# Kernel optimization log

Hardware: AMD Instinct MI355X
Metric: run time of the kernel (lower is better)

## Reference

```python
import jax, jax.numpy as jnp
import numpy as np

B, S, DIN, DK, DV = 8, 2048, 1024, 1024, 1024


def setup_inputs() -> dict:
    key = jax.random.key(0)
    ks = jax.random.split(key, 9)
    s_in = 1.0 / np.sqrt(DIN)
    return {
        "query": jax.random.normal(ks[0], (B, S, DIN), jnp.float32),
        "key_": jax.random.normal(ks[1], (B, S, DIN), jnp.float32),
        "value": jax.random.normal(ks[2], (B, S, DIN), jnp.float32),
        "Wq_w": jax.random.uniform(ks[3], (DK, DIN), jnp.float32, -s_in, s_in),
        "Wq_b": jax.random.uniform(ks[4], (DK,), jnp.float32, -s_in, s_in),
        "Wk_w": jax.random.uniform(ks[5], (DK, DIN), jnp.float32, -s_in, s_in),
        "Wk_b": jax.random.uniform(ks[6], (DK,), jnp.float32, -s_in, s_in),
        "Wv_w": jax.random.uniform(ks[7], (DV, DIN), jnp.float32, -s_in, s_in),
        "Wv_b": jax.random.uniform(ks[8], (DV,), jnp.float32, -s_in, s_in),
    }


def reference(query, key_, value, Wq_w, Wq_b, Wk_w, Wk_b, Wv_w, Wv_b):
    # Linear projections: x @ W.T + b (torch nn.Linear convention)
    Q = jnp.einsum('bsd,kd->bsk', query, Wq_w) + Wq_b   # [B,S,DK]
    K = jnp.einsum('bsd,kd->bsk', key_, Wk_w) + Wk_b    # [B,S,DK]
    V = jnp.einsum('bsd,vd->bsv', value, Wv_w) + Wv_b   # [B,S,DV]
    scale = 1.0 / jnp.sqrt(jnp.asarray(Q.shape[-1], Q.dtype))
    scores = jnp.einsum('bqk,bsk->bqs', Q, K) * scale   # [B,S,S]
    attn = jax.nn.softmax(scores, axis=-1)
    return jnp.einsum('bqs,bsv->bqv', attn, V)          # [B,S,DV]
```

## Files before the change

### kernel.cpp

```cpp
#include <hip/hip_runtime.h>

typedef unsigned short u16;
typedef float    f32x4  __attribute__((ext_vector_type(4)));
typedef __bf16   bf16x8 __attribute__((ext_vector_type(8)));
typedef u16      u16x4  __attribute__((ext_vector_type(4)));
typedef u16      u16x8  __attribute__((ext_vector_type(8)));

#define NB   8
#define NS   2048
#define ND   1024

__device__ __forceinline__ u16 f2bf(float x) {
    union { float f; unsigned u; } v; v.f = x;
    unsigned r = v.u + 0x7fffu + ((v.u >> 16) & 1u);
    return (u16)(r >> 16);
}
__device__ __forceinline__ float bf2f(u16 x) {
    union { unsigned u; float f; } v; v.u = ((unsigned)x) << 16;
    return v.f;
}

__global__ __launch_bounds__(256) void cvt_f32_bf16(const float* __restrict__ in,
                                                    u16* __restrict__ out, int n4) {
    int i = blockIdx.x * 256 + threadIdx.x;
    if (i >= n4) return;
    f32x4 v = ((const f32x4*)in)[i];
    u16x4 o;
    o[0] = f2bf(v[0]); o[1] = f2bf(v[1]); o[2] = f2bf(v[2]); o[3] = f2bf(v[3]);
    ((u16x4*)out)[i] = o;
}

template<int OUT_BF16, int BIAS>
__global__ __launch_bounds__(256, 2)
void gemm_bt_kernel(const u16* __restrict__ A, long long sA, int lda,
                    const u16* __restrict__ B, long long sB, int ldb,
                    void* __restrict__ Cv, long long sC, int ldc,
                    const float* __restrict__ bias, int K)
{
    __shared__ alignas(16) u16 ldsA[128 * 32];
    __shared__ alignas(16) u16 ldsB[128 * 32];
    const int z = blockIdx.z;
    A += sA * z;
    B += sB * z;
    const int t = threadIdx.x;
    const int w = t >> 6, l = t & 63;
    const int row0 = blockIdx.y * 128, col0 = blockIdx.x * 128;
    const int wr = (w >> 1) << 6, wc = (w & 1) << 6;

    f32x4 acc[4][4] = {};
    const int lr = l & 15, lk = (l >> 4) << 3;

    for (int kt = 0; kt < K; kt += 32) {
#pragma unroll
        for (int i = 0; i < 2; ++i) {
            const int c  = (i << 8) + t;
            const int r  = c >> 2;
            const int k8 = (c & 3) << 3;
            const u16* ga = A + (long long)(row0 + r) * lda + (kt + k8);
            const u16* gb = B + (long long)(col0 + r) * ldb + (kt + k8);
            u16* la = &ldsA[((i << 8) + (w << 6)) << 3];
            u16* lb = &ldsB[((i << 8) + (w << 6)) << 3];
            __builtin_amdgcn_global_load_lds((__attribute__((address_space(1))) void*)ga,
                                             (__attribute__((address_space(3))) void*)la, 16, 0, 0);
            __builtin_amdgcn_global_load_lds((__attribute__((address_space(1))) void*)gb,
                                             (__attribute__((address_space(3))) void*)lb, 16, 0, 0);
        }
        __syncthreads();

        bf16x8 af[4], bfr[4];
#pragma unroll
        for (int m = 0; m < 4; ++m)
            af[m] = *(const bf16x8*)&ldsA[(wr + (m << 4) + lr) * 32 + lk];
#pragma unroll
        for (int n = 0; n < 4; ++n)
            bfr[n] = *(const bf16x8*)&ldsB[(wc + (n << 4) + lr) * 32 + lk];
#pragma unroll
        for (int m = 0; m < 4; ++m)
#pragma unroll
            for (int n = 0; n < 4; ++n)
                acc[m][n] = __builtin_amdgcn_mfma_f32_16x16x32_bf16(af[m], bfr[n], acc[m][n], 0, 0, 0);
        __syncthreads();
    }

    const int fr = l & 15, fq = (l >> 4) << 2;
    u16*   Cb = (u16*)Cv + sC * z;
    float* Cf = (float*)Cv + sC * z;
#pragma unroll
    for (int m = 0; m < 4; ++m) {
#pragma unroll
        for (int n = 0; n < 4; ++n) {
#pragma unroll
            for (int j = 0; j < 4; ++j) {
                const int r  = row0 + wr + (m << 4) + fq + j;
                const int cc = col0 + wc + (n << 4) + fr;
                float vv = acc[m][n][j];
                if (BIAS == 1) vv += bias[cc];
                else if (BIAS == 2) vv += bias[r];
                if (OUT_BF16) Cb[(long long)r * ldc + cc] = f2bf(vv);
                else          Cf[(long long)r * ldc + cc] = vv;
            }
        }
    }
}

__global__ __launch_bounds__(256, 4)
void softmax_kernel(u16* __restrict__ sc, float scale2) {
    u16* row = sc + (long long)blockIdx.x * NS;
    const int t = threadIdx.x;
    u16x8 a = ((const u16x8*)row)[t];
    float x[8];
#pragma unroll
    for (int j = 0; j < 8; ++j) x[j] = bf2f(a[j]);
    float m = x[0];
#pragma unroll
    for (int j = 1; j < 8; ++j) m = fmaxf(m, x[j]);
#pragma unroll
    for (int off = 1; off < 64; off <<= 1) m = fmaxf(m, __shfl_xor(m, off));
    __shared__ float red[2][4];
    const int w = t >> 6;
    if ((t & 63) == 0) red[0][w] = m;
    __syncthreads();
    m = fmaxf(fmaxf(red[0][0], red[0][1]), fmaxf(red[0][2], red[0][3]));
    float e[8], s = 0.f;
#pragma unroll
    for (int j = 0; j < 8; ++j) { e[j] = exp2f((x[j] - m) * scale2); s += e[j]; }
#pragma unroll
    for (int off = 1; off < 64; off <<= 1) s += __shfl_xor(s, off);
    if ((t & 63) == 0) red[1][w] = s;
    __syncthreads();
    s = red[1][0] + red[1][1] + red[1][2] + red[1][3];
    const float inv = 1.0f / s;
    u16x8 o;
#pragma unroll
    for (int j = 0; j < 8; ++j) o[j] = f2bf(e[j] * inv);
    ((u16x8*)row)[t] = o;
}

extern "C" void kernel_launch(void* const* d_in, const int* in_sizes, int n_in,
                              void* d_out, int out_size, void* d_ws, size_t ws_size,
                              hipStream_t stream) {
    const float* q  = (const float*)d_in[0];
    const float* k  = (const float*)d_in[1];
    const float* v  = (const float*)d_in[2];
    const float* wq = (const float*)d_in[3];
    const float* bq = (const float*)d_in[4];
    const float* wk = (const float*)d_in[5];
    const float* bk = (const float*)d_in[6];
    const float* wv = (const float*)d_in[7];
    const float* bv = (const float*)d_in[8];
    float* out = (float*)d_out;

    char* ws = (char*)d_ws;
    const long long NIN = (long long)NB * NS * ND;
    const long long NW  = (long long)ND * ND;
    const long long NSC = (long long)NB * NS * NS;

    u16* SCB = (u16*)ws;
    u16* X   = (u16*)ws;
    u16* W   = X + NIN;
    u16* QB  = SCB + NSC;
    u16* KB  = QB + NIN;
    u16* VT  = KB + NIN;
    (void)ws_size; (void)in_sizes; (void)n_in; (void)out_size;

    cvt_f32_bf16<<<16384, 256, 0, stream>>>(q,  X, (int)(NIN / 4));
    cvt_f32_bf16<<<1024,  256, 0, stream>>>(wq, W, (int)(NW / 4));
    gemm_bt_kernel<1, 1><<<dim3(8, 128, 1), 256, 0, stream>>>(
        X, 0, ND, W, 0, ND, QB, 0, ND, bq, ND);

    cvt_f32_bf16<<<16384, 256, 0, stream>>>(k,  X, (int)(NIN / 4));
    cvt_f32_bf16<<<1024,  256, 0, stream>>>(wk, W, (int)(NW / 4));
    gemm_bt_kernel<1, 1><<<dim3(8, 128, 1), 256, 0, stream>>>(
        X, 0, ND, W, 0, ND, KB, 0, ND, bk, ND);

    cvt_f32_bf16<<<16384, 256, 0, stream>>>(v,  X, (int)(NIN / 4));
    cvt_f32_bf16<<<1024,  256, 0, stream>>>(wv, W, (int)(NW / 4));
    gemm_bt_kernel<1, 2><<<dim3(16, 8, NB), 256, 0, stream>>>(
        W, 0, ND, X, (long long)NS * ND, ND, VT, (long long)ND * NS, NS, bv, ND);

    gemm_bt_kernel<1, 0><<<dim3(16, 16, NB), 256, 0, stream>>>(
        QB, (long long)NS * ND, ND, KB, (long long)NS * ND, ND,
        SCB, (long long)NS * NS, NS, nullptr, ND);

    const float scale2 = (1.0f / 32.0f) * 1.44269504088896f;
    softmax_kernel<<<NB * NS, 256, 0, stream>>>(SCB, scale2);

    gemm_bt_kernel<0, 0><<<dim3(8, 16, NB), 256, 0, stream>>>(
        SCB, (long long)NS * NS, NS,
        VT, (long long)ND * NS, NS,
        out, (long long)NS * ND, ND, nullptr, NS);
}
```

Baseline: 601.2 us.

## Rewrite GEMM as 256x256-tile kernel with triple-buffered async LDS pipeline

Replaces the 128x128 single-buffered GEMM with a 512-thread kernel computing 256x256 tiles. Global-to-LDS loads go into three buffers so loads for later K steps overlap with MFMA on the current one. It also XOR-swizzles the LDS layout to avoid bank conflicts, remaps workgroup IDs for cache locality, and raises wave priority around the MFMA block. The larger tiles raise arithmetic intensity but need 96KB of LDS and more accumulator registers. Fewer workgroups per GEMM may also hurt tail balance.

Result: faster. 506.8 us (-15.7%).

```diff
diff --git a/kernel.cpp b/kernel.cpp
--- a/kernel.cpp
+++ b/kernel.cpp
@@ -31,73 +31,108 @@
 }
 
 template<int OUT_BF16, int BIAS>
-__global__ __launch_bounds__(256, 2)
-void gemm_bt_kernel(const u16* __restrict__ A, long long sA, int lda,
+__global__ __launch_bounds__(512, 2)
+void gemm256_kernel(const u16* __restrict__ A, long long sA, int lda,
                     const u16* __restrict__ B, long long sB, int ldb,
                     void* __restrict__ Cv, long long sC, int ldc,
                     const float* __restrict__ bias, int K)
 {
-    __shared__ alignas(16) u16 ldsA[128 * 32];
-    __shared__ alignas(16) u16 ldsB[128 * 32];
-    const int z = blockIdx.z;
-    A += sA * z;
-    B += sB * z;
+    __shared__ alignas(16) u16 lds[49152];
+
+    const int gx = gridDim.x, gy = gridDim.y;
+    const int nwg = gx * gy * (int)gridDim.z;
+    const int lin = blockIdx.x + gx * (blockIdx.y + gy * blockIdx.z);
+    const int chunk = nwg >> 3;
+    const int swz = (lin & 7) * chunk + (lin >> 3);
+    const int bx = swz % gx;
+    const int tq = swz / gx;
+    const int by = tq % gy;
+    const int bz = tq / gy;
+
+    A += sA * bz;
+    B += sB * bz;
+
+    const int row0 = by << 8, col0 = bx << 8;
     const int t = threadIdx.x;
     const int w = t >> 6, l = t & 63;
-    const int row0 = blockIdx.y * 128, col0 = blockIdx.x * 128;
-    const int wr = (w >> 1) << 6, wc = (w & 1) << 6;
-
-    f32x4 acc[4][4] = {};
-    const int lr = l & 15, lk = (l >> 4) << 3;
-
-    for (int kt = 0; kt < K; kt += 32) {
-#pragma unroll
-        for (int i = 0; i < 2; ++i) {
-            const int c  = (i << 8) + t;
-            const int r  = c >> 2;
-            const int k8 = (c & 3) << 3;
-            const u16* ga = A + (long long)(row0 + r) * lda + (kt + k8);
-            const u16* gb = B + (long long)(col0 + r) * ldb + (kt + k8);
-            u16* la = &ldsA[((i << 8) + (w << 6)) << 3];
-            u16* lb = &ldsB[((i << 8) + (w << 6)) << 3];
-            __builtin_amdgcn_global_load_lds((__attribute__((address_space(1))) void*)ga,
-                                             (__attribute__((address_space(3))) void*)la, 16, 0, 0);
-            __builtin_amdgcn_global_load_lds((__attribute__((address_space(1))) void*)gb,
-                                             (__attribute__((address_space(3))) void*)lb, 16, 0, 0);
+    const int wm = w >> 2, wn = w & 3;
+
+    const int j0e = ((l & 3) ^ ((l >> 3) & 3)) << 3;
+    const u16* gA0 = A + (long long)(row0 + (w << 4) + (l >> 2)) * lda + j0e;
+    const u16* gA1 = gA0 + ((long long)lda << 7);
+    const u16* gB0 = B + (long long)(col0 + (w << 4) + (l >> 2)) * ldb + j0e;
+    const u16* gB1 = gB0 + ((long long)ldb << 7);
+    const unsigned dA0 = (unsigned)(w << 10);
+
+    auto STAGE = [&](int buf, int kt) {
+        const unsigned bo = (unsigned)buf * 32768u;
+        __builtin_amdgcn_global_load_lds((__attribute__((address_space(1))) void*)(gA0 + kt),
+            (__attribute__((address_space(3))) void*)((char*)lds + bo + dA0),          16, 0, 0);
+        __builtin_amdgcn_global_load_lds((__attribute__((address_space(1))) void*)(gA1 + kt),
+            (__attribute__((address_space(3))) void*)((char*)lds + bo + dA0 + 8192),   16, 0, 0);
+        __builtin_amdgcn_global_load_lds((__attribute__((address_space(1))) void*)(gB0 + kt),
+            (__attribute__((address_space(3))) void*)((char*)lds + bo + 16384 + dA0),  16, 0, 0);
+        __builtin_amdgcn_global_load_lds((__attribute__((address_space(1))) void*)(gB1 + kt),
+            (__attribute__((address_space(3))) void*)((char*)lds + bo + 16384 + dA0 + 8192), 16, 0, 0);
+    };
+
+    const int lr  = l & 15;
+    const int jsw = ((l >> 4) ^ ((lr >> 1) & 3)) << 4;
+    const int aA  = ((wm << 7) + lr) * 64 + jsw;
+    const int aB  = 16384 + ((wn << 6) + lr) * 64 + jsw;
+
+    f32x4 acc[8][4] = {};
+    const int NT = K >> 5;
+
+    STAGE(0, 0);
+    STAGE(1, 32);
+
+    for (int tt = 0; tt < NT; ++tt) {
+        if (tt + 2 < NT) {
+            STAGE((tt + 2) % 3, (tt + 2) << 5);
+            asm volatile("s_waitcnt vmcnt(8)" ::: "memory");
+        } else if (tt + 1 < NT) {
+            asm volatile("s_waitcnt vmcnt(4)" ::: "memory");
+        } else {
+            asm volatile("s_waitcnt vmcnt(0)" ::: "memory");
         }
-        __syncthreads();
-
-        bf16x8 af[4], bfr[4];
-#pragma unroll
-        for (int m = 0; m < 4; ++m)
-            af[m] = *(const bf16x8*)&ldsA[(wr + (m << 4) + lr) * 32 + lk];
-#pragma unroll
-        for (int n = 0; n < 4; ++n)
-            bfr[n] = *(const bf16x8*)&ldsB[(wc + (n << 4) + lr) * 32 + lk];
-#pragma unroll
-        for (int m = 0; m < 4; ++m)
-#pragma unroll
-            for (int n = 0; n < 4; ++n)
-                acc[m][n] = __builtin_amdgcn_mfma_f32_16x16x32_bf16(af[m], bfr[n], acc[m][n], 0, 0, 0);
-        __syncthreads();
+        __builtin_amdgcn_s_barrier();
+
+        const char* bufp = (const char*)lds + (tt % 3) * 32768;
+        bf16x8 af[8], bfv[4];
+#pragma unroll
+        for (int mf = 0; mf < 8; ++mf) af[mf]  = *(const bf16x8*)(bufp + aA + mf * 1024);
+#pragma unroll
+        for (int nf = 0; nf < 4; ++nf) bfv[nf] = *(const bf16x8*)(bufp + aB + nf * 1024);
+
+        asm volatile("s_waitcnt lgkmcnt(0)" ::: "memory");
+        __builtin_amdgcn_s_barrier();
+
+        __builtin_amdgcn_s_setprio(1);
+#pragma unroll
+        for (int mf = 0; mf < 8; ++mf)
+#pragma unroll
+            for (int nf = 0; nf < 4; ++nf)
+                acc[mf][nf] = __builtin_amdgcn_mfma_f32_16x16x32_bf16(af[mf], bfv[nf], acc[mf][nf], 0, 0, 0);
+        __builtin_amdgcn_s_setprio(0);
     }
 
     const int fr = l & 15, fq = (l >> 4) << 2;
-    u16*   Cb = (u16*)Cv + sC * z;
-    float* Cf = (float*)Cv + sC * z;
-#pragma unroll
-    for (int m = 0; m < 4; ++m) {
-#pragma unroll
-        for (int n = 0; n < 4; ++n) {
+    u16*   Cb = (u16*)Cv + sC * bz;
+    float* Cf = (float*)Cv + sC * bz;
+#pragma unroll
+    for (int mf = 0; mf < 8; ++mf) {
+        const int r = row0 + (wm << 7) + (mf << 4) + fq;
+#pragma unroll
+        for (int nf = 0; nf < 4; ++nf) {
+            const int c = col0 + (wn << 6) + (nf << 4) + fr;
 #pragma unroll
             for (int j = 0; j < 4; ++j) {
-                const int r  = row0 + wr + (m << 4) + fq + j;
-                const int cc = col0 + wc + (n << 4) + fr;
-                float vv = acc[m][n][j];
-                if (BIAS == 1) vv += bias[cc];
-                else if (BIAS == 2) vv += bias[r];
-                if (OUT_BF16) Cb[(long long)r * ldc + cc] = f2bf(vv);
-                else          Cf[(long long)r * ldc + cc] = vv;
+                float vv = acc[mf][nf][j];
+                if (BIAS == 1) vv += bias[c];
+                else if (BIAS == 2) vv += bias[r + j];
+                if (OUT_BF16) Cb[(long long)(r + j) * ldc + c] = f2bf(vv);
+                else          Cf[(long long)(r + j) * ldc + c] = vv;
             }
         }
     }
@@ -165,27 +200,27 @@
 
     cvt_f32_bf16<<<16384, 256, 0, stream>>>(q,  X, (int)(NIN / 4));
     cvt_f32_bf16<<<1024,  256, 0, stream>>>(wq, W, (int)(NW / 4));
-    gemm_bt_kernel<1, 1><<<dim3(8, 128, 1), 256, 0, stream>>>(
+    gemm256_kernel<1, 1><<<dim3(4, 64, 1), 512, 0, stream>>>(
         X, 0, ND, W, 0, ND, QB, 0, ND, bq, ND);
 
     cvt_f32_bf16<<<16384, 256, 0, stream>>>(k,  X, (int)(NIN / 4));
     cvt_f32_bf16<<<1024,  256, 0, stream>>>(wk, W, (int)(NW / 4));
-    gemm_bt_kernel<1, 1><<<dim3(8, 128, 1), 256, 0, stream>>>(
+    gemm256_kernel<1, 1><<<dim3(4, 64, 1), 512, 0, stream>>>(
         X, 0, ND, W, 0, ND, KB, 0, ND, bk, ND);
 
     cvt_f32_bf16<<<16384, 256, 0, stream>>>(v,  X, (int)(NIN / 4));
     cvt_f32_bf16<<<1024,  256, 0, stream>>>(wv, W, (int)(NW / 4));
-    gemm_bt_kernel<1, 2><<<dim3(16, 8, NB), 256, 0, stream>>>(
+    gemm256_kernel<1, 2><<<dim3(8, 4, NB), 512, 0, stream>>>(
         W, 0, ND, X, (long long)NS * ND, ND, VT, (long long)ND * NS, NS, bv, ND);
 
-    gemm_bt_kernel<1, 0><<<dim3(16, 16, NB), 256, 0, stream>>>(
+    gemm256_kernel<1, 0><<<dim3(8, 8, NB), 512, 0, stream>>>(
         QB, (long long)NS * ND, ND, KB, (long long)NS * ND, ND,
         SCB, (long long)NS * NS, NS, nullptr, ND);
 
     const float scale2 = (1.0f / 32.0f) * 1.44269504088896f;
     softmax_kernel<<<NB * NS, 256, 0, stream>>>(SCB, scale2);
 
-    gemm_bt_kernel<0, 0><<<dim3(8, 16, NB), 256, 0, stream>>>(
+    gemm256_kernel<0, 0><<<dim3(4, 8, NB), 512, 0, stream>>>(
         SCB, (long long)NS * NS, NS,
         VT, (long long)ND * NS, NS,
         out, (long long)NS * ND, ND, nullptr, NS);
```
